# Optimization experiments

Hardware: AMD Instinct MI355X
Metric: run time of the kernel (lower is better)

Reference implementation:

```python
import jax, jax.numpy as jnp
import numpy as np
from jax import lax

# 5x5 Gaussian kernel, sigma=1.0 (matches cv2.getGaussianKernel(5, 1.0))
_xs = np.arange(5) - 2
_k1 = np.exp(-(_xs ** 2) / 2.0)
_k1 = (_k1 / _k1.sum()).astype(np.float32)
_K2 = jnp.asarray(np.outer(_k1, _k1))  # [5,5]


def _blur(x):
    """Gaussian blur on [B,H,W] with BORDER_REFLECT_101 (cv2 default)."""
    xp = jnp.pad(x, ((0, 0), (2, 2), (2, 2)), mode='reflect')
    y = lax.conv_general_dilated(xp[:, None], _K2[None, None], (1, 1), 'VALID')
    return y[:, 0]


def _hist_entropy(noise):
    """Per-image 50-bin histogram entropy over range (-0.5, 0.5). noise: [B,H,W]."""
    def one(v):
        h, _ = jnp.histogram(v, bins=50, range=(-0.5, 0.5))
        h = h.astype(jnp.float32)
        p = h / (h.sum() + 1e-10)
        return -jnp.sum(p * jnp.log2(p + 1e-10))
    return jax.vmap(one)(noise.reshape(noise.shape[0], -1))


def _noise_features(x):
    # x: [B,3,H,W] float in [0,1]
    # gray path: quantize to uint8 (truncation), cv2 RGB2GRAY weights w/ rounding
    xq = jnp.floor(jnp.clip(x * 255.0, 0.0, 255.0))  # uint8 truncation
    gray = jnp.round(0.299 * xq[:, 0] + 0.587 * xq[:, 1] + 0.114 * xq[:, 2]) / 255.0
    noise = gray - _blur(gray)  # [B,H,W]
    local_var = jnp.var(noise, axis=(1, 2))
    noise_std = jnp.std(noise, axis=(1, 2))
    entropy = _hist_entropy(noise)
    # per-channel noise std on the float image (no quantization in original)
    B, C, H, W = x.shape
    ch = x.reshape(B * C, H, W)
    ch_noise = ch - _blur(ch)
    ch_std = jnp.std(ch_noise, axis=(1, 2)).reshape(B, C)
    return jnp.stack([local_var, noise_std, entropy], axis=1).astype(jnp.float32)\
        , ch_std


def setup_inputs() -> dict:
    key = jax.random.key(0)
    ks = jax.random.split(key, 5)
    B, H, W = 64, 512, 512
    x = jax.random.uniform(ks[0], (B, 3, H, W), dtype=jnp.float32)
    # torch Linear weights: [out, in], kaiming-uniform-ish init
    W1 = jax.random.uniform(ks[1], (32, 6), minval=-1, maxval=1) / np.sqrt(6)
    b1 = jax.random.uniform(ks[2], (32,), minval=-1, maxval=1) / np.sqrt(6)
    W2 = jax.random.uniform(ks[3], (64, 32), minval=-1, maxval=1) / np.sqrt(32)
    b2 = jax.random.uniform(ks[4], (64,), minval=-1, maxval=1) / np.sqrt(32)
    return {"x": x, "W1": W1, "b1": b1, "W2": W2, "b2": b2}


def reference(x, W1, b1, W2, b2):
    stats, ch_std = _noise_features(x)
    feats = jnp.concatenate([stats, ch_std], axis=1)  # [B,6]
    h = jax.nn.relu(feats @ W1.T + b1)  # dropout in eval mode = identity
    return jax.nn.relu(h @ W2.T + b2)
```

## Files before the change

### kernel.cpp

```cpp
#include <hip/hip_runtime.h>
#include <math.h>

#define HH 512
#define WW 512
#define NB 64
#define CH_STRIDE (HH*WW)
#define IMG_STRIDE (3*CH_STRIDE)

#define GK0 0.0544886846f
#define GK1 0.2442013419f
#define GK2 0.4026199468f

__device__ __forceinline__ float quant255(float v) {
    return floorf(fminf(fmaxf(__fmul_rn(v, 255.0f), 0.0f), 255.0f));
}
__device__ __forceinline__ float gray255(float qa, float qb, float qc) {
    return rintf(__fadd_rn(__fadd_rn(__fmul_rn(0.299f, qa), __fmul_rn(0.587f, qb)),
                           __fmul_rn(0.114f, qc)));
}

__global__ __launch_bounds__(256, 2)
void noise_main(const float* __restrict__ x, float* __restrict__ gsums,
                unsigned int* __restrict__ ghist)
{
    __shared__ unsigned int lhist[4][2][50];
    const int tid  = threadIdx.x;
    const int lane = tid & 63;
    const int wid  = tid >> 6;
    for (int i = tid; i < 400; i += 256) ((unsigned int*)lhist)[i] = 0u;
    __syncthreads();

    const int blk   = blockIdx.x;
    const int b     = blk >> 3;
    const int strip = (blk >> 2) & 1;
    const int cg    = blk & 3;
    const int chunk = cg * 4 + wid;
    const int R0    = chunk * 32;
    const int X0    = strip * 256;
    const int gcol  = X0 + lane * 4;

    const float* pa = x + (size_t)b * IMG_STRIDE;
    const float* pb = pa + CH_STRIDE;
    const float* pc = pb + CH_STRIDE;

    const bool eL = (lane == 0)  && (X0 != 0);
    const bool eR = (lane == 63) && (X0 == 0);

    float hrA[5][4], hrB[5][4], hrC[5][4], hrG[5][4];
    float d1A[4], d1B[4], d1C[4], d1G[4];
    float d2A[4], d2B[4], d2C[4], d2G[4];
    float sA=0.f,qA=0.f,sB=0.f,qB=0.f,sC=0.f,qC=0.f,sG=0.f,qG=0.f;

    float4 va = {0,0,0,0}, vb = {0,0,0,0}, vc = {0,0,0,0};
    float2 el_a = {0,0}, el_b = {0,0}, el_c = {0,0};
    float2 er_a = {0,0}, er_b = {0,0}, er_c = {0,0};
    float4 nva = {0,0,0,0}, nvb = {0,0,0,0}, nvc = {0,0,0,0};
    float2 nel_a = {0,0}, nel_b = {0,0}, nel_c = {0,0};
    float2 ner_a = {0,0}, ner_b = {0,0}, ner_c = {0,0};

#define LOADROW(T, VA_, VB_, VC_, ELA, ELB, ELC, ERA, ERB, ERC) do {            \
        int r_ = R0 - 2 + (T);                                                  \
        r_ = (r_ < 0) ? -r_ : ((r_ >= HH) ? (2*(HH-1) - r_) : r_);              \
        const int ro_ = r_ * WW;                                                \
        VA_ = *(const float4*)(pa + ro_ + gcol);                                \
        VB_ = *(const float4*)(pb + ro_ + gcol);                                \
        VC_ = *(const float4*)(pc + ro_ + gcol);                                \
        if (eL) {                                                               \
            ELA = *(const float2*)(pa + ro_ + 254);                             \
            ELB = *(const float2*)(pb + ro_ + 254);                             \
            ELC = *(const float2*)(pc + ro_ + 254);                             \
        }                                                                       \
        if (eR) {                                                               \
            ERA = *(const float2*)(pa + ro_ + 256);                             \
            ERB = *(const float2*)(pb + ro_ + 256);                             \
            ERC = *(const float2*)(pc + ro_ + 256);                             \
        }                                                                       \
    } while (0)

    LOADROW(0, va, vb, vc, el_a, el_b, el_c, er_a, er_b, er_c);

    #pragma unroll 1
    for (int tb = 0; tb < 8; ++tb) {
        #pragma unroll
        for (int u = 0; u < 5; ++u) {
            const int t = tb * 5 + u;
            if (t < 36) {
                if (t + 1 < 36)
                    LOADROW(t + 1, nva, nvb, nvc, nel_a, nel_b, nel_c, ner_a, ner_b, ner_c);

                float g0 = gray255(quant255(va.x), quant255(vb.x), quant255(vc.x));
                float g1 = gray255(quant255(va.y), quant255(vb.y), quant255(vc.y));
                float g2 = gray255(quant255(va.z), quant255(vb.z), quant255(vc.z));
                float g3 = gray255(quant255(va.w), quant255(vb.w), quant255(vc.w));

                float l2a = __shfl_up(va.z, 1), l1a = __shfl_up(va.w, 1);
                float l2b = __shfl_up(vb.z, 1), l1b = __shfl_up(vb.w, 1);
                float l2c = __shfl_up(vc.z, 1), l1c = __shfl_up(vc.w, 1);
                float r0a = __shfl_down(va.x, 1), r1a = __shfl_down(va.y, 1);
                float r0b = __shfl_down(vb.x, 1), r1b = __shfl_down(vb.y, 1);
                float r0c = __shfl_down(vc.x, 1), r1c = __shfl_down(vc.y, 1);
                float gl2 = __shfl_up(g2, 1),   gl1 = __shfl_up(g3, 1);
                float gr0 = __shfl_down(g0, 1), gr1 = __shfl_down(g1, 1);

                if (lane == 0) {
                    if (X0 == 0) {
                        l2a = va.z; l1a = va.y; l2b = vb.z; l1b = vb.y; l2c = vc.z; l1c = vc.y;
                        gl2 = g2;   gl1 = g1;
                    } else {
                        l2a = el_a.x; l1a = el_a.y; l2b = el_b.x; l1b = el_b.y; l2c = el_c.x; l1c = el_c.y;
                        gl2 = gray255(quant255(el_a.x), quant255(el_b.x), quant255(el_c.x));
                        gl1 = gray255(quant255(el_a.y), quant255(el_b.y), quant255(el_c.y));
                    }
                }
                if (lane == 63) {
                    if (X0 == 0) {
                        r0a = er_a.x; r1a = er_a.y; r0b = er_b.x; r1b = er_b.y; r0c = er_c.x; r1c = er_c.y;
                        gr0 = gray255(quant255(er_a.x), quant255(er_b.x), quant255(er_c.x));
                        gr1 = gray255(quant255(er_a.y), quant255(er_b.y), quant255(er_c.y));
                    } else {
                        r0a = va.z; r1a = va.y; r0b = vb.z; r1b = vb.y; r0c = vc.z; r1c = vc.y;
                        gr0 = g2;   gr1 = g1;
                    }
                }

                hrA[u][0] = GK0*(l2a+va.z) + GK1*(l1a+va.y) + GK2*va.x;
                hrA[u][1] = GK0*(l1a+va.w) + GK1*(va.x+va.z) + GK2*va.y;
                hrA[u][2] = GK0*(va.x+r0a) + GK1*(va.y+va.w) + GK2*va.z;
                hrA[u][3] = GK0*(va.y+r1a) + GK1*(va.z+r0a) + GK2*va.w;
                hrB[u][0] = GK0*(l2b+vb.z) + GK1*(l1b+vb.y) + GK2*vb.x;
                hrB[u][1] = GK0*(l1b+vb.w) + GK1*(vb.x+vb.z) + GK2*vb.y;
                hrB[u][2] = GK0*(vb.x+r0b) + GK1*(vb.y+vb.w) + GK2*vb.z;
                hrB[u][3] = GK0*(vb.y+r1b) + GK1*(vb.z+r0b) + GK2*vb.w;
                hrC[u][0] = GK0*(l2c+vc.z) + GK1*(l1c+vc.y) + GK2*vc.x;
                hrC[u][1] = GK0*(l1c+vc.w) + GK1*(vc.x+vc.z) + GK2*vc.y;
                hrC[u][2] = GK0*(vc.x+r0c) + GK1*(vc.y+vc.w) + GK2*vc.z;
                hrC[u][3] = GK0*(vc.y+r1c) + GK1*(vc.z+r0c) + GK2*vc.w;
                hrG[u][0] = GK0*(gl2+g2) + GK1*(gl1+g1) + GK2*g0;
                hrG[u][1] = GK0*(gl1+g3) + GK1*(g0+g2)  + GK2*g1;
                hrG[u][2] = GK0*(g0+gr0) + GK1*(g1+g3)  + GK2*g2;
                hrG[u][3] = GK0*(g1+gr1) + GK1*(g2+gr0) + GK2*g3;

                if (t >= 4) {
                    const int s0=(u+1)%5, s1=(u+2)%5, s2=(u+3)%5, s3=(u+4)%5, s4=u;
                    #pragma unroll
                    for (int j = 0; j < 4; ++j) {
                        float bl, v;
                        bl = GK0*(hrA[s0][j]+hrA[s4][j]) + GK1*(hrA[s1][j]+hrA[s3][j]) + GK2*hrA[s2][j];
                        v  = d2A[j] - bl;  sA += v;  qA = fmaf(v, v, qA);
                        bl = GK0*(hrB[s0][j]+hrB[s4][j]) + GK1*(hrB[s1][j]+hrB[s3][j]) + GK2*hrB[s2][j];
                        v  = d2B[j] - bl;  sB += v;  qB = fmaf(v, v, qB);
                        bl = GK0*(hrC[s0][j]+hrC[s4][j]) + GK1*(hrC[s1][j]+hrC[s3][j]) + GK2*hrC[s2][j];
                        v  = d2C[j] - bl;  sC += v;  qC = fmaf(v, v, qC);
                        bl = GK0*(hrG[s0][j]+hrG[s4][j]) + GK1*(hrG[s1][j]+hrG[s3][j]) + GK2*hrG[s2][j];
                        v  = d2G[j] - bl;  sG += v;  qG = fmaf(v, v, qG);
                        if (v >= -127.5f && v <= 127.5f) {
                            int idx = (int)((v + 127.5f) * 0.19607843137254902f);
                            idx = idx > 49 ? 49 : idx;
                            atomicAdd(&lhist[wid][lane & 1][idx], 1u);
                        }
                    }
                }

                #pragma unroll
                for (int j = 0; j < 4; ++j) { d2A[j]=d1A[j]; d2B[j]=d1B[j]; d2C[j]=d1C[j]; d2G[j]=d1G[j]; }
                d1A[0]=va.x; d1A[1]=va.y; d1A[2]=va.z; d1A[3]=va.w;
                d1B[0]=vb.x; d1B[1]=vb.y; d1B[2]=vb.z; d1B[3]=vb.w;
                d1C[0]=vc.x; d1C[1]=vc.y; d1C[2]=vc.z; d1C[3]=vc.w;
                d1G[0]=g0;   d1G[1]=g1;   d1G[2]=g2;   d1G[3]=g3;

                va = nva; vb = nvb; vc = nvc;
                el_a = nel_a; el_b = nel_b; el_c = nel_c;
                er_a = ner_a; er_b = ner_b; er_c = ner_c;
            }
        }
    }
#undef LOADROW

    float acc[8] = {sA, qA, sB, qB, sC, qC, sG, qG};
    #pragma unroll
    for (int f = 0; f < 8; ++f) {
        float v = acc[f];
        #pragma unroll
        for (int o = 32; o > 0; o >>= 1) v += __shfl_down(v, o);
        if (lane == 0) atomicAdd(&gsums[b*8 + f], v);
    }
    __syncthreads();
    if (tid < 50) {
        unsigned int h = 0;
        #pragma unroll
        for (int w = 0; w < 4; ++w) h += lhist[w][0][tid] + lhist[w][1][tid];
        atomicAdd(&ghist[b*50 + tid], h);
    }
}

__global__ __launch_bounds__(64)
void noise_final(const float* __restrict__ gsums, const unsigned int* __restrict__ ghist,
                 const float* __restrict__ W1, const float* __restrict__ b1,
                 const float* __restrict__ W2, const float* __restrict__ b2,
                 float* __restrict__ out)
{
    const int b = threadIdx.x;
    if (b >= NB) return;
    const float invN = 1.0f / (float)(HH*WW);
    float feats[6];
    {
        float s = gsums[b*8 + 6], q = gsums[b*8 + 7];
        float m = s * invN;
        float var255 = q * invN - m*m;
        var255 = var255 < 0.f ? 0.f : var255;
        float var = var255 * (1.0f/65025.0f);
        feats[0] = var; feats[1] = sqrtf(var);
    }
    {
        float tot = 0.f;
        for (int i = 0; i < 50; ++i) tot += (float)ghist[b*50 + i];
        float inv = 1.0f / (tot + 1e-10f);
        float e = 0.f;
        for (int i = 0; i < 50; ++i) {
            float p = (float)ghist[b*50 + i] * inv;
            e -= p * log2f(p + 1e-10f);
        }
        feats[2] = e;
    }
    for (int c = 0; c < 3; ++c) {
        float s = gsums[b*8 + 2*c], q = gsums[b*8 + 2*c + 1];
        float m = s * invN;
        float v = q * invN - m*m;
        feats[3+c] = sqrtf(v < 0.f ? 0.f : v);
    }
    float h[32];
    #pragma unroll
    for (int i = 0; i < 32; ++i) {
        float a = b1[i];
        #pragma unroll
        for (int j = 0; j < 6; ++j) a = fmaf(feats[j], W1[i*6 + j], a);
        h[i] = a > 0.f ? a : 0.f;
    }
    for (int k = 0; k < 64; ++k) {
        float a = b2[k];
        #pragma unroll
        for (int j = 0; j < 32; ++j) a = fmaf(h[j], W2[k*32 + j], a);
        out[b*64 + k] = a > 0.f ? a : 0.f;
    }
}

extern "C" void kernel_launch(void* const* d_in, const int* in_sizes, int n_in,
                              void* d_out, int out_size, void* d_ws, size_t ws_size,
                              hipStream_t stream) {
    (void)in_sizes; (void)n_in; (void)out_size; (void)ws_size;
    const float* x  = (const float*)d_in[0];
    const float* W1 = (const float*)d_in[1];
    const float* b1 = (const float*)d_in[2];
    const float* W2 = (const float*)d_in[3];
    const float* b2 = (const float*)d_in[4];
    float* out = (float*)d_out;

    float* gsums = (float*)d_ws;
    unsigned int* ghist = (unsigned int*)((char*)d_ws + NB*8*4);
    hipMemsetAsync(d_ws, 0, NB*8*4 + NB*50*4, stream);

    hipLaunchKernelGGL(noise_main, dim3(512), dim3(256), 0, stream, x, gsums, ghist);
    hipLaunchKernelGGL(noise_final, dim3(1), dim3(64), 0, stream,
                       gsums, ghist, W1, b1, W2, b2, out);
}
```

Measured before the change: 335.5 us.

## Halve per-thread column width, double grid, and interleave block-to-image mapping

Each thread now handles 2 columns instead of 4, the image is split into four 128-column strips, and the grid doubles to 1024 blocks with launch bounds allowing 4 blocks per SM. Block indices are permuted so that consecutive blocks land on different images and strips, which is meant to spread memory traffic across channels. The histogram privatisation widens from 2 to 4 copies per wave to cut LDS atomic contention. In exchange, each lane reads narrower float2 loads, a larger fraction of lanes sit on strip edges and need extra halo loads, and the halo shuffles are amortised over fewer outputs.

New measurement: 354.3 us. 1.06x slower.

```diff
diff --git a/kernel.cpp b/kernel.cpp
--- a/kernel.cpp
+++ b/kernel.cpp
@@ -16,68 +16,65 @@
 }
 __device__ __forceinline__ float gray255(float qa, float qb, float qc) {
     return rintf(__fadd_rn(__fadd_rn(__fmul_rn(0.299f, qa), __fmul_rn(0.587f, qb)),
-                           __fmul_rn(0.114f, qc)));
-}
-
-__global__ __launch_bounds__(256, 2)
+                           __fadd_rn(__fmul_rn(0.114f, qc), 0.0f)));
+}
+
+__global__ __launch_bounds__(256, 4)
 void noise_main(const float* __restrict__ x, float* __restrict__ gsums,
                 unsigned int* __restrict__ ghist)
 {
-    __shared__ unsigned int lhist[4][2][50];
+    __shared__ unsigned int lhist[4][4][50];
     const int tid  = threadIdx.x;
     const int lane = tid & 63;
     const int wid  = tid >> 6;
-    for (int i = tid; i < 400; i += 256) ((unsigned int*)lhist)[i] = 0u;
+    for (int i = tid; i < 800; i += 256) ((unsigned int*)lhist)[i] = 0u;
     __syncthreads();
 
-    const int blk   = blockIdx.x;
-    const int b     = blk >> 3;
-    const int strip = (blk >> 2) & 1;
+    const int rawblk = blockIdx.x;
+    const int blk = (rawblk & 7) * 128 + (rawblk >> 3);
+
+    const int b     = blk >> 4;
+    const int strip = (blk >> 2) & 3;
     const int cg    = blk & 3;
     const int chunk = cg * 4 + wid;
     const int R0    = chunk * 32;
-    const int X0    = strip * 256;
-    const int gcol  = X0 + lane * 4;
+    const int X0    = strip * 128;
+    const int gcol  = X0 + lane * 2;
 
     const float* pa = x + (size_t)b * IMG_STRIDE;
     const float* pb = pa + CH_STRIDE;
     const float* pc = pb + CH_STRIDE;
 
-    const bool eL = (lane == 0)  && (X0 != 0);
-    const bool eR = (lane == 63) && (X0 == 0);
-
-    float hrA[5][4], hrB[5][4], hrC[5][4], hrG[5][4];
-    float d1A[4], d1B[4], d1C[4], d1G[4];
-    float d2A[4], d2B[4], d2C[4], d2G[4];
+    const bool eL  = (lane == 0)  && (X0 != 0);
+    const bool eR  = (lane == 63) && (X0 != 384);
+    const bool eLR = eL || eR;
+    const int  ecol = eL ? (X0 - 2) : (X0 + 128);
+
+    float hrA[5][2], hrB[5][2], hrC[5][2], hrG[5][2];
+    float d1A[2], d1B[2], d1C[2], d1G[2];
+    float d2A[2], d2B[2], d2C[2], d2G[2];
     float sA=0.f,qA=0.f,sB=0.f,qB=0.f,sC=0.f,qC=0.f,sG=0.f,qG=0.f;
 
-    float4 va = {0,0,0,0}, vb = {0,0,0,0}, vc = {0,0,0,0};
-    float2 el_a = {0,0}, el_b = {0,0}, el_c = {0,0};
-    float2 er_a = {0,0}, er_b = {0,0}, er_c = {0,0};
-    float4 nva = {0,0,0,0}, nvb = {0,0,0,0}, nvc = {0,0,0,0};
-    float2 nel_a = {0,0}, nel_b = {0,0}, nel_c = {0,0};
-    float2 ner_a = {0,0}, ner_b = {0,0}, ner_c = {0,0};
-
-#define LOADROW(T, VA_, VB_, VC_, ELA, ELB, ELC, ERA, ERB, ERC) do {            \
+    float2 va = {0,0}, vb = {0,0}, vc = {0,0};
+    float2 e_a = {0,0}, e_b = {0,0}, e_c = {0,0};
+    float2 nva = {0,0}, nvb = {0,0}, nvc = {0,0};
+    float2 ne_a = {0,0}, ne_b = {0,0}, ne_c = {0,0};
+
+#define LOADROW(T, VA_, VB_, VC_, EA_, EB_, EC_) do {                           \
         int r_ = R0 - 2 + (T);                                                  \
         r_ = (r_ < 0) ? -r_ : ((r_ >= HH) ? (2*(HH-1) - r_) : r_);              \
         const int ro_ = r_ * WW;                                                \
-        VA_ = *(const float4*)(pa + ro_ + gcol);                                \
-        VB_ = *(const float4*)(pb + ro_ + gcol);                                \
-        VC_ = *(const float4*)(pc + ro_ + gcol);                                \
-        if (eL) {                                                               \
-            ELA = *(const float2*)(pa + ro_ + 254);                             \
-            ELB = *(const float2*)(pb + ro_ + 254);                             \
-            ELC = *(const float2*)(pc + ro_ + 254);                             \
-        }                                                                       \
-        if (eR) {                                                               \
-            ERA = *(const float2*)(pa + ro_ + 256);                             \
-            ERB = *(const float2*)(pb + ro_ + 256);                             \
-            ERC = *(const float2*)(pc + ro_ + 256);                             \
+        VA_ = *(const float2*)(pa + ro_ + gcol);                                \
+        VB_ = *(const float2*)(pb + ro_ + gcol);                                \
+        VC_ = *(const float2*)(pc + ro_ + gcol);                                \
+        if (eLR) {                                                              \
+            EA_ = *(const float2*)(pa + ro_ + ecol);                            \
+            EB_ = *(const float2*)(pb + ro_ + ecol);                            \
+            EC_ = *(const float2*)(pc + ro_ + ecol);                            \
         }                                                                       \
     } while (0)
 
-    LOADROW(0, va, vb, vc, el_a, el_b, el_c, er_a, er_b, er_c);
+    LOADROW(0, va, vb, vc, e_a, e_b, e_c);
 
     #pragma unroll 1
     for (int tb = 0; tb < 8; ++tb) {
@@ -86,64 +83,54 @@
             const int t = tb * 5 + u;
             if (t < 36) {
                 if (t + 1 < 36)
-                    LOADROW(t + 1, nva, nvb, nvc, nel_a, nel_b, nel_c, ner_a, ner_b, ner_c);
+                    LOADROW(t + 1, nva, nvb, nvc, ne_a, ne_b, ne_c);
 
                 float g0 = gray255(quant255(va.x), quant255(vb.x), quant255(vc.x));
                 float g1 = gray255(quant255(va.y), quant255(vb.y), quant255(vc.y));
-                float g2 = gray255(quant255(va.z), quant255(vb.z), quant255(vc.z));
-                float g3 = gray255(quant255(va.w), quant255(vb.w), quant255(vc.w));
-
-                float l2a = __shfl_up(va.z, 1), l1a = __shfl_up(va.w, 1);
-                float l2b = __shfl_up(vb.z, 1), l1b = __shfl_up(vb.w, 1);
-                float l2c = __shfl_up(vc.z, 1), l1c = __shfl_up(vc.w, 1);
+
+                float l2a = __shfl_up(va.x, 1), l1a = __shfl_up(va.y, 1);
+                float l2b = __shfl_up(vb.x, 1), l1b = __shfl_up(vb.y, 1);
+                float l2c = __shfl_up(vc.x, 1), l1c = __shfl_up(vc.y, 1);
                 float r0a = __shfl_down(va.x, 1), r1a = __shfl_down(va.y, 1);
                 float r0b = __shfl_down(vb.x, 1), r1b = __shfl_down(vb.y, 1);
                 float r0c = __shfl_down(vc.x, 1), r1c = __shfl_down(vc.y, 1);
-                float gl2 = __shfl_up(g2, 1),   gl1 = __shfl_up(g3, 1);
+                float gl2 = __shfl_up(g0, 1),   gl1 = __shfl_up(g1, 1);
                 float gr0 = __shfl_down(g0, 1), gr1 = __shfl_down(g1, 1);
 
                 if (lane == 0) {
                     if (X0 == 0) {
-                        l2a = va.z; l1a = va.y; l2b = vb.z; l1b = vb.y; l2c = vc.z; l1c = vc.y;
-                        gl2 = g2;   gl1 = g1;
+                        l2a = r0a; l1a = va.y; l2b = r0b; l1b = vb.y; l2c = r0c; l1c = vc.y;
+                        gl2 = gr0; gl1 = g1;
                     } else {
-                        l2a = el_a.x; l1a = el_a.y; l2b = el_b.x; l1b = el_b.y; l2c = el_c.x; l1c = el_c.y;
-                        gl2 = gray255(quant255(el_a.x), quant255(el_b.x), quant255(el_c.x));
-                        gl1 = gray255(quant255(el_a.y), quant255(el_b.y), quant255(el_c.y));
+                        l2a = e_a.x; l1a = e_a.y; l2b = e_b.x; l1b = e_b.y; l2c = e_c.x; l1c = e_c.y;
+                        gl2 = gray255(quant255(e_a.x), quant255(e_b.x), quant255(e_c.x));
+                        gl1 = gray255(quant255(e_a.y), quant255(e_b.y), quant255(e_c.y));
                     }
                 }
                 if (lane == 63) {
-                    if (X0 == 0) {
-                        r0a = er_a.x; r1a = er_a.y; r0b = er_b.x; r1b = er_b.y; r0c = er_c.x; r1c = er_c.y;
-                        gr0 = gray255(quant255(er_a.x), quant255(er_b.x), quant255(er_c.x));
-                        gr1 = gray255(quant255(er_a.y), quant255(er_b.y), quant255(er_c.y));
+                    if (X0 != 384) {
+                        r0a = e_a.x; r1a = e_a.y; r0b = e_b.x; r1b = e_b.y; r0c = e_c.x; r1c = e_c.y;
+                        gr0 = gray255(quant255(e_a.x), quant255(e_b.x), quant255(e_c.x));
+                        gr1 = gray255(quant255(e_a.y), quant255(e_b.y), quant255(e_c.y));
                     } else {
-                        r0a = va.z; r1a = va.y; r0b = vb.z; r1b = vb.y; r0c = vc.z; r1c = vc.y;
-                        gr0 = g2;   gr1 = g1;
+                        r0a = va.x; r1a = l1a; r0b = vb.x; r1b = l1b; r0c = vc.x; r1c = l1c;
+                        gr0 = g0;   gr1 = gl1;
                     }
                 }
 
-                hrA[u][0] = GK0*(l2a+va.z) + GK1*(l1a+va.y) + GK2*va.x;
-                hrA[u][1] = GK0*(l1a+va.w) + GK1*(va.x+va.z) + GK2*va.y;
-                hrA[u][2] = GK0*(va.x+r0a) + GK1*(va.y+va.w) + GK2*va.z;
-                hrA[u][3] = GK0*(va.y+r1a) + GK1*(va.z+r0a) + GK2*va.w;
-                hrB[u][0] = GK0*(l2b+vb.z) + GK1*(l1b+vb.y) + GK2*vb.x;
-                hrB[u][1] = GK0*(l1b+vb.w) + GK1*(vb.x+vb.z) + GK2*vb.y;
-                hrB[u][2] = GK0*(vb.x+r0b) + GK1*(vb.y+vb.w) + GK2*vb.z;
-                hrB[u][3] = GK0*(vb.y+r1b) + GK1*(vb.z+r0b) + GK2*vb.w;
-                hrC[u][0] = GK0*(l2c+vc.z) + GK1*(l1c+vc.y) + GK2*vc.x;
-                hrC[u][1] = GK0*(l1c+vc.w) + GK1*(vc.x+vc.z) + GK2*vc.y;
-                hrC[u][2] = GK0*(vc.x+r0c) + GK1*(vc.y+vc.w) + GK2*vc.z;
-                hrC[u][3] = GK0*(vc.y+r1c) + GK1*(vc.z+r0c) + GK2*vc.w;
-                hrG[u][0] = GK0*(gl2+g2) + GK1*(gl1+g1) + GK2*g0;
-                hrG[u][1] = GK0*(gl1+g3) + GK1*(g0+g2)  + GK2*g1;
-                hrG[u][2] = GK0*(g0+gr0) + GK1*(g1+g3)  + GK2*g2;
-                hrG[u][3] = GK0*(g1+gr1) + GK1*(g2+gr0) + GK2*g3;
+                hrA[u][0] = GK0*(l2a+r0a) + GK1*(l1a+va.y) + GK2*va.x;
+                hrA[u][1] = GK0*(l1a+r1a) + GK1*(va.x+r0a) + GK2*va.y;
+                hrB[u][0] = GK0*(l2b+r0b) + GK1*(l1b+vb.y) + GK2*vb.x;
+                hrB[u][1] = GK0*(l1b+r1b) + GK1*(vb.x+r0b) + GK2*vb.y;
+                hrC[u][0] = GK0*(l2c+r0c) + GK1*(l1c+vc.y) + GK2*vc.x;
+                hrC[u][1] = GK0*(l1c+r1c) + GK1*(vc.x+r0c) + GK2*vc.y;
+                hrG[u][0] = GK0*(gl2+gr0) + GK1*(gl1+g1)  + GK2*g0;
+                hrG[u][1] = GK0*(gl1+gr1) + GK1*(g0+gr0)  + GK2*g1;
 
                 if (t >= 4) {
                     const int s0=(u+1)%5, s1=(u+2)%5, s2=(u+3)%5, s3=(u+4)%5, s4=u;
                     #pragma unroll
-                    for (int j = 0; j < 4; ++j) {
+                    for (int j = 0; j < 2; ++j) {
                         float bl, v;
                         bl = GK0*(hrA[s0][j]+hrA[s4][j]) + GK1*(hrA[s1][j]+hrA[s3][j]) + GK2*hrA[s2][j];
                         v  = d2A[j] - bl;  sA += v;  qA = fmaf(v, v, qA);
@@ -156,21 +143,20 @@
                         if (v >= -127.5f && v <= 127.5f) {
                             int idx = (int)((v + 127.5f) * 0.19607843137254902f);
                             idx = idx > 49 ? 49 : idx;
-                            atomicAdd(&lhist[wid][lane & 1][idx], 1u);
+                            atomicAdd(&lhist[wid][lane & 3][idx], 1u);
                         }
                     }
                 }
 
                 #pragma unroll
-                for (int j = 0; j < 4; ++j) { d2A[j]=d1A[j]; d2B[j]=d1B[j]; d2C[j]=d1C[j]; d2G[j]=d1G[j]; }
-                d1A[0]=va.x; d1A[1]=va.y; d1A[2]=va.z; d1A[3]=va.w;
-                d1B[0]=vb.x; d1B[1]=vb.y; d1B[2]=vb.z; d1B[3]=vb.w;
-                d1C[0]=vc.x; d1C[1]=vc.y; d1C[2]=vc.z; d1C[3]=vc.w;
-                d1G[0]=g0;   d1G[1]=g1;   d1G[2]=g2;   d1G[3]=g3;
+                for (int j = 0; j < 2; ++j) { d2A[j]=d1A[j]; d2B[j]=d1B[j]; d2C[j]=d1C[j]; d2G[j]=d1G[j]; }
+                d1A[0]=va.x; d1A[1]=va.y;
+                d1B[0]=vb.x; d1B[1]=vb.y;
+                d1C[0]=vc.x; d1C[1]=vc.y;
+                d1G[0]=g0;   d1G[1]=g1;
 
                 va = nva; vb = nvb; vc = nvc;
-                el_a = nel_a; el_b = nel_b; el_c = nel_c;
-                er_a = ner_a; er_b = ner_b; er_c = ner_c;
+                e_a = ne_a; e_b = ne_b; e_c = ne_c;
             }
         }
     }
@@ -188,7 +174,9 @@
     if (tid < 50) {
         unsigned int h = 0;
         #pragma unroll
-        for (int w = 0; w < 4; ++w) h += lhist[w][0][tid] + lhist[w][1][tid];
+        for (int w = 0; w < 4; ++w)
+            #pragma unroll
+            for (int p = 0; p < 4; ++p) h += lhist[w][p][tid];
         atomicAdd(&ghist[b*50 + tid], h);
     }
 }
@@ -259,7 +247,7 @@
     unsigned int* ghist = (unsigned int*)((char*)d_ws + NB*8*4);
     hipMemsetAsync(d_ws, 0, NB*8*4 + NB*50*4, stream);
 
-    hipLaunchKernelGGL(noise_main, dim3(512), dim3(256), 0, stream, x, gsums, ghist);
+    hipLaunchKernelGGL(noise_main, dim3(1024), dim3(256), 0, stream, x, gsums, ghist);
     hipLaunchKernelGGL(noise_final, dim3(1), dim3(64), 0, stream,
                        gsums, ghist, W1, b1, W2, b2, out);
 }
```

## Halve rows per wave, double grid, swizzle block order, widen histogram privatization

Applied to the files above, without the earlier changes.

Each wave now handles 16 output rows instead of 32, so the grid doubles to 1024 blocks and launch bounds target 4 blocks per CU for higher occupancy. Block indices are remapped so that consecutive blocks are spread across images and row groups. The shared histogram is replicated four ways per wave to reduce atomic contention, and the left/right edge loads share one code path. The cost is more halo reloading: each 16-row chunk reads 20 rows instead of 36 per 32 rows, and register pressure is tighter under the new bounds.

Result: slower. 665.3 us (+98.3%).

```diff
diff --git a/kernel.cpp b/kernel.cpp
--- a/kernel.cpp
+++ b/kernel.cpp
@@ -19,23 +19,25 @@
                            __fmul_rn(0.114f, qc)));
 }
 
-__global__ __launch_bounds__(256, 2)
+__global__ __launch_bounds__(256, 4)
 void noise_main(const float* __restrict__ x, float* __restrict__ gsums,
                 unsigned int* __restrict__ ghist)
 {
-    __shared__ unsigned int lhist[4][2][50];
+    __shared__ unsigned int lhist[4][4][50];
     const int tid  = threadIdx.x;
     const int lane = tid & 63;
     const int wid  = tid >> 6;
-    for (int i = tid; i < 400; i += 256) ((unsigned int*)lhist)[i] = 0u;
+    for (int i = tid; i < 800; i += 256) ((unsigned int*)lhist)[i] = 0u;
     __syncthreads();
 
-    const int blk   = blockIdx.x;
-    const int b     = blk >> 3;
-    const int strip = (blk >> 2) & 1;
-    const int cg    = blk & 3;
+    const int rawblk = blockIdx.x;
+    const int blk = (rawblk & 7) * 128 + (rawblk >> 3);
+
+    const int b     = blk >> 4;
+    const int strip = (blk >> 3) & 1;
+    const int cg    = blk & 7;
     const int chunk = cg * 4 + wid;
-    const int R0    = chunk * 32;
+    const int R0    = chunk * 16;
     const int X0    = strip * 256;
     const int gcol  = X0 + lane * 4;
 
@@ -43,135 +45,127 @@
     const float* pb = pa + CH_STRIDE;
     const float* pc = pb + CH_STRIDE;
 
-    const bool eL = (lane == 0)  && (X0 != 0);
-    const bool eR = (lane == 63) && (X0 == 0);
+    const bool eL  = (lane == 0)  && (X0 != 0);
+    const bool eR  = (lane == 63) && (X0 == 0);
+    const bool eLR = eL || eR;
+    const int  ecol = eL ? 254 : 256;
 
     float hrA[5][4], hrB[5][4], hrC[5][4], hrG[5][4];
-    float d1A[4], d1B[4], d1C[4], d1G[4];
-    float d2A[4], d2B[4], d2C[4], d2G[4];
+    float d1A[4]={0,0,0,0}, d1B[4]={0,0,0,0}, d1C[4]={0,0,0,0}, d1G[4]={0,0,0,0};
+    float d2A[4]={0,0,0,0}, d2B[4]={0,0,0,0}, d2C[4]={0,0,0,0}, d2G[4]={0,0,0,0};
     float sA=0.f,qA=0.f,sB=0.f,qB=0.f,sC=0.f,qC=0.f,sG=0.f,qG=0.f;
 
     float4 va = {0,0,0,0}, vb = {0,0,0,0}, vc = {0,0,0,0};
-    float2 el_a = {0,0}, el_b = {0,0}, el_c = {0,0};
-    float2 er_a = {0,0}, er_b = {0,0}, er_c = {0,0};
+    float2 e_a = {0,0}, e_b = {0,0}, e_c = {0,0};
     float4 nva = {0,0,0,0}, nvb = {0,0,0,0}, nvc = {0,0,0,0};
-    float2 nel_a = {0,0}, nel_b = {0,0}, nel_c = {0,0};
-    float2 ner_a = {0,0}, ner_b = {0,0}, ner_c = {0,0};
-
-#define LOADROW(T, VA_, VB_, VC_, ELA, ELB, ELC, ERA, ERB, ERC) do {            \
+    float2 ne_a = {0,0}, ne_b = {0,0}, ne_c = {0,0};
+
+#define LOADROW(T, VA_, VB_, VC_, EA_, EB_, EC_) do {                           \
         int r_ = R0 - 2 + (T);                                                  \
         r_ = (r_ < 0) ? -r_ : ((r_ >= HH) ? (2*(HH-1) - r_) : r_);              \
         const int ro_ = r_ * WW;                                                \
         VA_ = *(const float4*)(pa + ro_ + gcol);                                \
         VB_ = *(const float4*)(pb + ro_ + gcol);                                \
         VC_ = *(const float4*)(pc + ro_ + gcol);                                \
-        if (eL) {                                                               \
-            ELA = *(const float2*)(pa + ro_ + 254);                             \
-            ELB = *(const float2*)(pb + ro_ + 254);                             \
-            ELC = *(const float2*)(pc + ro_ + 254);                             \
-        }                                                                       \
-        if (eR) {                                                               \
-            ERA = *(const float2*)(pa + ro_ + 256);                             \
-            ERB = *(const float2*)(pb + ro_ + 256);                             \
-            ERC = *(const float2*)(pc + ro_ + 256);                             \
+        if (eLR) {                                                              \
+            EA_ = *(const float2*)(pa + ro_ + ecol);                            \
+            EB_ = *(const float2*)(pb + ro_ + ecol);                            \
+            EC_ = *(const float2*)(pc + ro_ + ecol);                            \
         }                                                                       \
     } while (0)
 
-    LOADROW(0, va, vb, vc, el_a, el_b, el_c, er_a, er_b, er_c);
+    LOADROW(0, va, vb, vc, e_a, e_b, e_c);
 
     #pragma unroll 1
-    for (int tb = 0; tb < 8; ++tb) {
+    for (int tb = 0; tb < 4; ++tb) {
         #pragma unroll
         for (int u = 0; u < 5; ++u) {
             const int t = tb * 5 + u;
-            if (t < 36) {
-                if (t + 1 < 36)
-                    LOADROW(t + 1, nva, nvb, nvc, nel_a, nel_b, nel_c, ner_a, ner_b, ner_c);
-
-                float g0 = gray255(quant255(va.x), quant255(vb.x), quant255(vc.x));
-                float g1 = gray255(quant255(va.y), quant255(vb.y), quant255(vc.y));
-                float g2 = gray255(quant255(va.z), quant255(vb.z), quant255(vc.z));
-                float g3 = gray255(quant255(va.w), quant255(vb.w), quant255(vc.w));
-
-                float l2a = __shfl_up(va.z, 1), l1a = __shfl_up(va.w, 1);
-                float l2b = __shfl_up(vb.z, 1), l1b = __shfl_up(vb.w, 1);
-                float l2c = __shfl_up(vc.z, 1), l1c = __shfl_up(vc.w, 1);
-                float r0a = __shfl_down(va.x, 1), r1a = __shfl_down(va.y, 1);
-                float r0b = __shfl_down(vb.x, 1), r1b = __shfl_down(vb.y, 1);
-                float r0c = __shfl_down(vc.x, 1), r1c = __shfl_down(vc.y, 1);
-                float gl2 = __shfl_up(g2, 1),   gl1 = __shfl_up(g3, 1);
-                float gr0 = __shfl_down(g0, 1), gr1 = __shfl_down(g1, 1);
-
-                if (lane == 0) {
-                    if (X0 == 0) {
-                        l2a = va.z; l1a = va.y; l2b = vb.z; l1b = vb.y; l2c = vc.z; l1c = vc.y;
-                        gl2 = g2;   gl1 = g1;
-                    } else {
-                        l2a = el_a.x; l1a = el_a.y; l2b = el_b.x; l1b = el_b.y; l2c = el_c.x; l1c = el_c.y;
-                        gl2 = gray255(quant255(el_a.x), quant255(el_b.x), quant255(el_c.x));
-                        gl1 = gray255(quant255(el_a.y), quant255(el_b.y), quant255(el_c.y));
+            if (t + 1 < 20)
+                LOADROW(t + 1, nva, nvb, nvc, ne_a, ne_b, ne_c);
+
+            float g0 = gray255(quant255(va.x), quant255(vb.x), quant255(vc.x));
+            float g1 = gray255(quant255(va.y), quant255(vb.y), quant255(vc.y));
+            float g2 = gray255(quant255(va.z), quant255(vb.z), quant255(vc.z));
+            float g3 = gray255(quant255(va.w), quant255(vb.w), quant255(vc.w));
+
+            float l2a = __shfl_up(va.z, 1), l1a = __shfl_up(va.w, 1);
+            float l2b = __shfl_up(vb.z, 1), l1b = __shfl_up(vb.w, 1);
+            float l2c = __shfl_up(vc.z, 1), l1c = __shfl_up(vc.w, 1);
+            float r0a = __shfl_down(va.x, 1), r1a = __shfl_down(va.y, 1);
+            float r0b = __shfl_down(vb.x, 1), r1b = __shfl_down(vb.y, 1);
+            float r0c = __shfl_down(vc.x, 1), r1c = __shfl_down(vc.y, 1);
+            float gl2 = __shfl_up(g2, 1),   gl1 = __shfl_up(g3, 1);
+            float gr0 = __shfl_down(g0, 1), gr1 = __shfl_down(g1, 1);
+
+            if (lane == 0) {
+                if (X0 == 0) {
+                    l2a = va.z; l1a = va.y; l2b = vb.z; l1b = vb.y; l2c = vc.z; l1c = vc.y;
+                    gl2 = g2;   gl1 = g1;
+                } else {
+                    l2a = e_a.x; l1a = e_a.y; l2b = e_b.x; l1b = e_b.y; l2c = e_c.x; l1c = e_c.y;
+                    gl2 = gray255(quant255(e_a.x), quant255(e_b.x), quant255(e_c.x));
+                    gl1 = gray255(quant255(e_a.y), quant255(e_b.y), quant255(e_c.y));
+                }
+            }
+            if (lane == 63) {
+                if (X0 == 0) {
+                    r0a = e_a.x; r1a = e_a.y; r0b = e_b.x; r1b = e_b.y; r0c = e_c.x; r1c = e_c.y;
+                    gr0 = gray255(quant255(e_a.x), quant255(e_b.x), quant255(e_c.x));
+                    gr1 = gray255(quant255(e_a.y), quant255(e_b.y), quant255(e_c.y));
+                } else {
+                    r0a = va.z; r1a = va.y; r0b = vb.z; r1b = vb.y; r0c = vc.z; r1c = vc.y;
+                    gr0 = g2;   gr1 = g1;
+                }
+            }
+
+            hrA[u][0] = GK0*(l2a+va.z) + GK1*(l1a+va.y) + GK2*va.x;
+            hrA[u][1] = GK0*(l1a+va.w) + GK1*(va.x+va.z) + GK2*va.y;
+            hrA[u][2] = GK0*(va.x+r0a) + GK1*(va.y+va.w) + GK2*va.z;
+            hrA[u][3] = GK0*(va.y+r1a) + GK1*(va.z+r0a) + GK2*va.w;
+            hrB[u][0] = GK0*(l2b+vb.z) + GK1*(l1b+vb.y) + GK2*vb.x;
+            hrB[u][1] = GK0*(l1b+vb.w) + GK1*(vb.x+vb.z) + GK2*vb.y;
+            hrB[u][2] = GK0*(vb.x+r0b) + GK1*(vb.y+vb.w) + GK2*vb.z;
+            hrB[u][3] = GK0*(vb.y+r1b) + GK1*(vb.z+r0b) + GK2*vb.w;
+            hrC[u][0] = GK0*(l2c+vc.z) + GK1*(l1c+vc.y) + GK2*vc.x;
+            hrC[u][1] = GK0*(l1c+vc.w) + GK1*(vc.x+vc.z) + GK2*vc.y;
+            hrC[u][2] = GK0*(vc.x+r0c) + GK1*(vc.y+vc.w) + GK2*vc.z;
+            hrC[u][3] = GK0*(vc.y+r1c) + GK1*(vc.z+r0c) + GK2*vc.w;
+            hrG[u][0] = GK0*(gl2+g2) + GK1*(gl1+g1) + GK2*g0;
+            hrG[u][1] = GK0*(gl1+g3) + GK1*(g0+g2)  + GK2*g1;
+            hrG[u][2] = GK0*(g0+gr0) + GK1*(g1+g3)  + GK2*g2;
+            hrG[u][3] = GK0*(g1+gr1) + GK1*(g2+gr0) + GK2*g3;
+
+            if (t >= 4) {
+                const int s0=(u+1)%5, s1=(u+2)%5, s2=(u+3)%5, s3=(u+4)%5, s4=u;
+                #pragma unroll
+                for (int j = 0; j < 4; ++j) {
+                    float bl, v;
+                    bl = GK0*(hrA[s0][j]+hrA[s4][j]) + GK1*(hrA[s1][j]+hrA[s3][j]) + GK2*hrA[s2][j];
+                    v  = d2A[j] - bl;  sA += v;  qA = fmaf(v, v, qA);
+                    bl = GK0*(hrB[s0][j]+hrB[s4][j]) + GK1*(hrB[s1][j]+hrB[s3][j]) + GK2*hrB[s2][j];
+                    v  = d2B[j] - bl;  sB += v;  qB = fmaf(v, v, qB);
+                    bl = GK0*(hrC[s0][j]+hrC[s4][j]) + GK1*(hrC[s1][j]+hrC[s3][j]) + GK2*hrC[s2][j];
+                    v  = d2C[j] - bl;  sC += v;  qC = fmaf(v, v, qC);
+                    bl = GK0*(hrG[s0][j]+hrG[s4][j]) + GK1*(hrG[s1][j]+hrG[s3][j]) + GK2*hrG[s2][j];
+                    v  = d2G[j] - bl;  sG += v;  qG = fmaf(v, v, qG);
+                    if (v >= -127.5f && v <= 127.5f) {
+                        int idx = (int)((v + 127.5f) * 0.19607843137254902f);
+                        idx = idx > 49 ? 49 : idx;
+                        atomicAdd(&lhist[wid][lane & 3][idx], 1u);
                     }
                 }
-                if (lane == 63) {
-                    if (X0 == 0) {
-                        r0a = er_a.x; r1a = er_a.y; r0b = er_b.x; r1b = er_b.y; r0c = er_c.x; r1c = er_c.y;
-                        gr0 = gray255(quant255(er_a.x), quant255(er_b.x), quant255(er_c.x));
-                        gr1 = gray255(quant255(er_a.y), quant255(er_b.y), quant255(er_c.y));
-                    } else {
-                        r0a = va.z; r1a = va.y; r0b = vb.z; r1b = vb.y; r0c = vc.z; r1c = vc.y;
-                        gr0 = g2;   gr1 = g1;
-                    }
-                }
-
-                hrA[u][0] = GK0*(l2a+va.z) + GK1*(l1a+va.y) + GK2*va.x;
-                hrA[u][1] = GK0*(l1a+va.w) + GK1*(va.x+va.z) + GK2*va.y;
-                hrA[u][2] = GK0*(va.x+r0a) + GK1*(va.y+va.w) + GK2*va.z;
-                hrA[u][3] = GK0*(va.y+r1a) + GK1*(va.z+r0a) + GK2*va.w;
-                hrB[u][0] = GK0*(l2b+vb.z) + GK1*(l1b+vb.y) + GK2*vb.x;
-                hrB[u][1] = GK0*(l1b+vb.w) + GK1*(vb.x+vb.z) + GK2*vb.y;
-                hrB[u][2] = GK0*(vb.x+r0b) + GK1*(vb.y+vb.w) + GK2*vb.z;
-                hrB[u][3] = GK0*(vb.y+r1b) + GK1*(vb.z+r0b) + GK2*vb.w;
-                hrC[u][0] = GK0*(l2c+vc.z) + GK1*(l1c+vc.y) + GK2*vc.x;
-                hrC[u][1] = GK0*(l1c+vc.w) + GK1*(vc.x+vc.z) + GK2*vc.y;
-                hrC[u][2] = GK0*(vc.x+r0c) + GK1*(vc.y+vc.w) + GK2*vc.z;
-                hrC[u][3] = GK0*(vc.y+r1c) + GK1*(vc.z+r0c) + GK2*vc.w;
-                hrG[u][0] = GK0*(gl2+g2) + GK1*(gl1+g1) + GK2*g0;
-                hrG[u][1] = GK0*(gl1+g3) + GK1*(g0+g2)  + GK2*g1;
-                hrG[u][2] = GK0*(g0+gr0) + GK1*(g1+g3)  + GK2*g2;
-                hrG[u][3] = GK0*(g1+gr1) + GK1*(g2+gr0) + GK2*g3;
-
-                if (t >= 4) {
-                    const int s0=(u+1)%5, s1=(u+2)%5, s2=(u+3)%5, s3=(u+4)%5, s4=u;
-                    #pragma unroll
-                    for (int j = 0; j < 4; ++j) {
-                        float bl, v;
-                        bl = GK0*(hrA[s0][j]+hrA[s4][j]) + GK1*(hrA[s1][j]+hrA[s3][j]) + GK2*hrA[s2][j];
-                        v  = d2A[j] - bl;  sA += v;  qA = fmaf(v, v, qA);
-                        bl = GK0*(hrB[s0][j]+hrB[s4][j]) + GK1*(hrB[s1][j]+hrB[s3][j]) + GK2*hrB[s2][j];
-                        v  = d2B[j] - bl;  sB += v;  qB = fmaf(v, v, qB);
-                        bl = GK0*(hrC[s0][j]+hrC[s4][j]) + GK1*(hrC[s1][j]+hrC[s3][j]) + GK2*hrC[s2][j];
-                        v  = d2C[j] - bl;  sC += v;  qC = fmaf(v, v, qC);
-                        bl = GK0*(hrG[s0][j]+hrG[s4][j]) + GK1*(hrG[s1][j]+hrG[s3][j]) + GK2*hrG[s2][j];
-                        v  = d2G[j] - bl;  sG += v;  qG = fmaf(v, v, qG);
-                        if (v >= -127.5f && v <= 127.5f) {
-                            int idx = (int)((v + 127.5f) * 0.19607843137254902f);
-                            idx = idx > 49 ? 49 : idx;
-                            atomicAdd(&lhist[wid][lane & 1][idx], 1u);
-                        }
-                    }
-                }
-
-                #pragma unroll
-                for (int j = 0; j < 4; ++j) { d2A[j]=d1A[j]; d2B[j]=d1B[j]; d2C[j]=d1C[j]; d2G[j]=d1G[j]; }
-                d1A[0]=va.x; d1A[1]=va.y; d1A[2]=va.z; d1A[3]=va.w;
-                d1B[0]=vb.x; d1B[1]=vb.y; d1B[2]=vb.z; d1B[3]=vb.w;
-                d1C[0]=vc.x; d1C[1]=vc.y; d1C[2]=vc.z; d1C[3]=vc.w;
-                d1G[0]=g0;   d1G[1]=g1;   d1G[2]=g2;   d1G[3]=g3;
-
-                va = nva; vb = nvb; vc = nvc;
-                el_a = nel_a; el_b = nel_b; el_c = nel_c;
-                er_a = ner_a; er_b = ner_b; er_c = ner_c;
             }
+
+            #pragma unroll
+            for (int j = 0; j < 4; ++j) { d2A[j]=d1A[j]; d2B[j]=d1B[j]; d2C[j]=d1C[j]; d2G[j]=d1G[j]; }
+            d1A[0]=va.x; d1A[1]=va.y; d1A[2]=va.z; d1A[3]=va.w;
+            d1B[0]=vb.x; d1B[1]=vb.y; d1B[2]=vb.z; d1B[3]=vb.w;
+            d1C[0]=vc.x; d1C[1]=vc.y; d1C[2]=vc.z; d1C[3]=vc.w;
+            d1G[0]=g0;   d1G[1]=g1;   d1G[2]=g2;   d1G[3]=g3;
+
+            va = nva; vb = nvb; vc = nvc;
+            e_a = ne_a; e_b = ne_b; e_c = ne_c;
         }
     }
 #undef LOADROW
@@ -188,7 +182,9 @@
     if (tid < 50) {
         unsigned int h = 0;
         #pragma unroll
-        for (int w = 0; w < 4; ++w) h += lhist[w][0][tid] + lhist[w][1][tid];
+        for (int w = 0; w < 4; ++w)
+            #pragma unroll
+            for (int p = 0; p < 4; ++p) h += lhist[w][p][tid];
         atomicAdd(&ghist[b*50 + tid], h);
     }
 }
@@ -259,7 +255,7 @@
     unsigned int* ghist = (unsigned int*)((char*)d_ws + NB*8*4);
     hipMemsetAsync(d_ws, 0, NB*8*4 + NB*50*4, stream);
 
-    hipLaunchKernelGGL(noise_main, dim3(512), dim3(256), 0, stream, x, gsums, ghist);
+    hipLaunchKernelGGL(noise_main, dim3(1024), dim3(256), 0, stream, x, gsums, ghist);
     hipLaunchKernelGGL(noise_final, dim3(1), dim3(64), 0, stream,
                        gsums, ghist, W1, b1, W2, b2, out);
 }
```
